# Kernel tuning notes

Hardware: AMD Instinct MI355X
Metric: run time of the kernel (lower is better)

## Reference

```python
import jax, jax.numpy as jnp
import numpy as np

PAD, BOS, EOS, UNK = 0, 1, 2, 3
B, S, V, D, L = 256, 512, 50000, 256, 128

def setup_inputs() -> dict:
    key = jax.random.key(0)
    ks = jax.random.split(key, 12)
    vocab_tensor = jax.random.randint(ks[0], (B, S), 4, V)
    parent_idx = jax.random.randint(ks[1], (B, S), 0, S)
    pbond = jax.random.randint(ks[2], (B, S), 0, 4)
    bond = jax.random.randint(ks[3], (B, S), 0, 4)
    patom = jax.random.randint(ks[4], (B, S), 0, 16)
    atom = jax.random.randint(ks[5], (B, S), 0, 16)
    btype = jax.random.randint(ks[6], (B, S), 0, 4)
    order_tensor = jnp.stack([parent_idx, pbond, bond, patom, atom, btype], axis=-1)
    lengths = jax.random.randint(ks[7], (B,), 1, S + 1)
    mask_tensor = jnp.arange(S)[None, :] < lengths[:, None]  # ragged prefix masks
    eps = jax.random.normal(ks[8], (B, L), dtype=jnp.float32)
    sc = 1.0 / np.sqrt(D)
    emb = jax.random.normal(ks[9], (V, D), dtype=jnp.float32) * sc
    Wm = jax.random.normal(ks[10], (D, L), dtype=jnp.float32) * sc
    Wv = jax.random.normal(ks[11], (D, L), dtype=jnp.float32) * sc
    Wlin = jax.random.normal(jax.random.fold_in(key, 20), (L, D), dtype=jnp.float32) / np.sqrt(L)
    Wout = jax.random.normal(jax.random.fold_in(key, 21), (D, D), dtype=jnp.float32) * sc
    return {
        'vocab_tensor': vocab_tensor, 'order_tensor': order_tensor, 'mask_tensor': mask_tensor,
        'eps': eps, 'emb': emb, 'Wm': Wm, 'bm': jnp.zeros((L,), jnp.float32),
        'Wv': Wv, 'bv': jnp.zeros((L,), jnp.float32), 'Wlin': Wlin,
        'blin': jnp.zeros((D,), jnp.float32), 'Wout': Wout, 'bout': jnp.zeros((D,), jnp.float32),
    }

def _forward(vocab_tensor, order_tensor, mask_tensor, eps, emb, Wm, bm, Wv, bv, Wlin, blin, Wout, bout):
    # --- mask bond-pos columns (torch.where assignments, vectorized) ---
    # (columns 1 and 2 set to -1 where masked; kept implicitly via vt/pad handling)
    # --- calc_chem_z path: masked vocab, parent gather, edge one-hot ---
    vt = jnp.where(mask_tensor, vocab_tensor, PAD)                      # [B,S]
    vocab_emb = emb[vt]                                                 # [B,S,D]
    oi = order_tensor[..., 0]
    oi = jnp.where(oi == -1, BOS, oi)
    parent = jnp.where(mask_tensor, jnp.take_along_axis(vt, oi, axis=1), PAD)
    parent = parent.at[:, 0].set(BOS)
    parent_emb = emb[parent]                                            # [B,S,D]
    idx = jnp.clip(order_tensor[..., 5] - 1, -1, None)
    edge_type = jnp.where((idx >= 0)[..., None],
                          jax.nn.one_hot(jnp.clip(idx, 0), 3, dtype=jnp.float32), 0.0)  # [B,S,3]
    # pooling stand-in for (undefined) StructureEncoder -> [B,D]
    m = mask_tensor[..., None].astype(jnp.float32)
    enc = ((vocab_emb + parent_emb) * m).sum(1) / jnp.maximum(m.sum(1), 1.0)
    enc = enc * (1.0 + 0.0 * edge_type.sum())  # keep edge_type in graph
    # --- LatentSampler ---
    mean = enc @ Wm + bm
    log_var = enc @ Wv + bv
    z = mean + eps * jnp.exp(0.5 * log_var)
    memory = z @ Wlin + blin                                            # [B,D]
    # --- vectorized bos/eos/pad sequence assembly (the hot loop in torch) ---
    inp = jnp.concatenate([jnp.full((B, 1), BOS, vocab_tensor.dtype), vocab_tensor], axis=1)  # [B,S+1]
    mask_ex = jnp.concatenate([jnp.ones((B, 1), bool), mask_tensor], axis=1)
    tgt = jnp.roll(inp, -1, axis=1)
    first_false = jnp.argmax(~mask_ex, axis=1)                          # first eos position
    has_false = jnp.any(~mask_ex, axis=1)
    pos = jnp.arange(S + 1)[None, :]
    tgt = jnp.where(has_false[:, None] & (pos == first_false[:, None] - 1), EOS, tgt)
    kill = has_false[:, None] & (pos >= first_false[:, None])
    tgt = jnp.where(kill, PAD, tgt)
    inp = jnp.where(kill, PAD, inp)
    # edge_index assembly (faithful, consumed by decoder in original)
    padneg = jnp.full((B, 1), -1, order_tensor.dtype)
    edge_index = jnp.concatenate([padneg, jnp.where(mask_tensor, order_tensor[..., 0], -2) + 1], axis=1)
    # --- embedding lookups + decoder stand-in + output head ---
    node_embed = emb[inp]                                               # [B,S+1,D]
    dec = node_embed + memory[:, None, :]
    dec = dec + 0.0 * edge_index[..., None].astype(jnp.float32)         # keep edge_index in graph
    word_emb = dec @ Wout + bout
    tgt_emb = emb[tgt]
    valid = (tgt != PAD)
    sq = (word_emb - tgt_emb) ** 2 * valid[..., None]
    token_loss = sq.sum() / jnp.maximum(valid.sum() * D, 1).astype(jnp.float32)
    kl = -0.5 * jnp.sum(1.0 + log_var - mean ** 2 - jnp.exp(log_var)) / B
    return token_loss, kl

def reference(vocab_tensor, order_tensor, mask_tensor, eps, emb, Wm, bm, Wv, bv, Wlin, blin, Wout, bout):
    return _forward(vocab_tensor, order_tensor, mask_tensor, eps, emb, Wm, bm, Wv, bv, Wlin, blin, Wout, bout)
```

## Files before the change

kernel.cpp:

```cpp
#include <hip/hip_runtime.h>

#define B_ 256
#define S_ 512
#define V_ 50000
#define D_ 256
#define L_ 128
#define PGRID 512

typedef __attribute__((ext_vector_type(8))) short short8;
typedef __attribute__((ext_vector_type(4))) float floatx4;

#define OFF_SQP  16
#define OFF_WT   (OFF_SQP + 256)
#define OFF_EB   (OFF_WT + 32768)
#define OFF_P    (OFF_EB + (V_ * D_ / 2))

__device__ __forceinline__ unsigned short f2bf(float x) {
    unsigned u = __float_as_uint(x);
    u += 0x7FFFu + ((u >> 16) & 1u);
    return (unsigned short)(u >> 16);
}
__device__ __forceinline__ float bf2f(unsigned short u) {
    return __uint_as_float(((unsigned)u) << 16);
}

__global__ __launch_bounds__(256) void prep_kernel(const float* __restrict__ emb,
                                                   const float* __restrict__ Wout,
                                                   unsigned short* __restrict__ embb,
                                                   unsigned short* __restrict__ Wt,
                                                   float* __restrict__ ws) {
    __shared__ float sT[64][65];
    const int tid = threadIdx.x;
    if (blockIdx.x == 0) {
        if (tid < 16) ((int*)ws)[tid] = 0;
        ws[OFF_SQP + tid] = 0.f;
    }
    if (blockIdx.x < 16) {
        const int bx = blockIdx.x;
        const int k0 = (bx & 3) * 64, n0 = (bx >> 2) * 64;
        const int c = tid & 63, rg = tid >> 6;
#pragma unroll
        for (int i = 0; i < 16; ++i) {
            int r = rg * 16 + i;
            sT[c][r] = Wout[(k0 + r) * D_ + n0 + c];
        }
        __syncthreads();
#pragma unroll
        for (int i = 0; i < 16; ++i) {
            int r = rg * 16 + i;
            Wt[(size_t)(n0 + r) * D_ + k0 + c] = f2bf(sT[r][c]);
        }
    }
    const int N4 = V_ * D_ / 4;
    for (int i = blockIdx.x * 256 + tid; i < N4; i += gridDim.x * 256) {
        float4 v = ((const float4*)emb)[i];
        ushort4 h;
        h.x = f2bf(v.x); h.y = f2bf(v.y); h.z = f2bf(v.z); h.w = f2bf(v.w);
        ((ushort4*)embb)[i] = h;
    }
}

__global__ __launch_bounds__(256, 2) void pgemm_kernel(
    const unsigned short* __restrict__ embb, const unsigned short* __restrict__ Wt,
    unsigned short* __restrict__ P) {
    const int tid = threadIdx.x;
    const int wv = tid >> 6, lane = tid & 63;
    const int lo = lane & 15, hi = lane >> 4;
    const int NCH = V_ / 16;

    short8 bfr[4][8];
    const unsigned short* wbase = Wt + (size_t)(wv * 64 + lo) * D_ + hi * 8;
#pragma unroll
    for (int nt = 0; nt < 4; ++nt)
#pragma unroll
        for (int kk = 0; kk < 8; ++kk)
            bfr[nt][kk] = *(const short8*)(wbase + nt * 16 * D_ + kk * 32);

    int ch = blockIdx.x;
    const unsigned short* abase = embb + (size_t)(ch * 16 + lo) * D_ + hi * 8;
    short8 acur[8];
#pragma unroll
    for (int kk = 0; kk < 8; ++kk) acur[kk] = *(const short8*)(abase + kk * 32);

    for (; ch < NCH; ch += PGRID) {
        const int chn = (ch + PGRID < NCH) ? (ch + PGRID) : ch;
        const unsigned short* anext = embb + (size_t)(chn * 16 + lo) * D_ + hi * 8;
        short8 anxt[8];
#pragma unroll
        for (int kk = 0; kk < 8; ++kk) anxt[kk] = *(const short8*)(anext + kk * 32);

        floatx4 acc[4];
#pragma unroll
        for (int nt = 0; nt < 4; ++nt) acc[nt] = (floatx4){0.f, 0.f, 0.f, 0.f};
#pragma unroll
        for (int kk = 0; kk < 8; ++kk)
#pragma unroll
            for (int nt = 0; nt < 4; ++nt)
                acc[nt] = __builtin_amdgcn_mfma_f32_16x16x32_bf16(
                    acur[kk], bfr[nt][kk], acc[nt], 0, 0, 0);

#pragma unroll
        for (int r = 0; r < 4; ++r) {
            unsigned short* prow = P + (size_t)(ch * 16 + hi * 4 + r) * D_ + wv * 64 + lo;
#pragma unroll
            for (int nt = 0; nt < 4; ++nt) prow[nt * 16] = f2bf(acc[nt][r]);
        }
#pragma unroll
        for (int kk = 0; kk < 8; ++kk) acur[kk] = anxt[kk];
    }
}

__global__ __launch_bounds__(1024) void enclat_kernel(
    const int* __restrict__ vocab, const int* __restrict__ order,
    const int* __restrict__ mask, const unsigned short* __restrict__ embb,
    const unsigned short* __restrict__ P, const float* __restrict__ eps,
    const float* __restrict__ Wm, const float* __restrict__ bm,
    const float* __restrict__ Wv, const float* __restrict__ bv,
    const float* __restrict__ Wlin, const float* __restrict__ blin,
    const float* __restrict__ Wout, const float* __restrict__ bout,
    float* __restrict__ ws, float* __restrict__ out) {
    __shared__ int s_id1[S_], s_id2[S_];
    __shared__ float4 s_part[15 * 64];
    __shared__ float s_enc[D_];
    __shared__ float s_mean[L_], s_lv[L_], s_z[L_], s_mem[D_], s_Q[D_];
    __shared__ float s_red[256];
    __shared__ float s_wred[16];
    __shared__ int s_cnt, s_prev;
    const int b = blockIdx.x;
    const int tid = threadIdx.x;
    float* kl_acc = ws + 1;
    int* vc_acc = (int*)ws + 2;
    int* done = (int*)ws + 3;
    float* sqp = ws + OFF_SQP;

    if (tid == 0) s_cnt = 0;
    __syncthreads();
    if (tid < S_) {
        int j = tid;
        int mk = mask[b * S_ + j];
        int id1 = 0, id2 = 0;
        if (mk) {
            id1 = vocab[b * S_ + j];
            if (j == 0) {
                id2 = 1;
            } else {
                int oi = order[(size_t)(b * S_ + j) * 6];
                if (oi == -1) oi = 1;
                id2 = mask[b * S_ + oi] ? vocab[b * S_ + oi] : 0;
            }
        }
        s_id1[j] = id1;
        s_id2[j] = id2;
        unsigned long long bal = __ballot(mk != 0);
        if ((tid & 63) == 0) atomicAdd(&s_cnt, __popcll(bal));
    }
    __syncthreads();
    const int cnt = s_cnt;
    const int jg = tid >> 6, d4 = tid & 63;
    const ushort4* eb4 = (const ushort4*)embb;
    float4 a = {0.f, 0.f, 0.f, 0.f};
#pragma unroll 8
    for (int j = jg; j < cnt; j += 16) {
        ushort4 x = eb4[(size_t)s_id1[j] * 64 + d4];
        ushort4 y = eb4[(size_t)s_id2[j] * 64 + d4];
        a.x += bf2f(x.x) + bf2f(y.x);
        a.y += bf2f(x.y) + bf2f(y.y);
        a.z += bf2f(x.z) + bf2f(y.z);
        a.w += bf2f(x.w) + bf2f(y.w);
    }
    if (jg) s_part[(jg - 1) * 64 + d4] = a;
    __syncthreads();
    if (jg == 0) {
#pragma unroll
        for (int g = 0; g < 15; ++g) {
            float4 p = s_part[g * 64 + d4];
            a.x += p.x; a.y += p.y; a.z += p.z; a.w += p.w;
        }
        float inv = 1.f / fmaxf((float)cnt, 1.f);
        a.x *= inv; a.y *= inv; a.z *= inv; a.w *= inv;
        ((float4*)s_enc)[d4] = a;
    }
    __syncthreads();
    float dot = 0.f;
    if (tid < 256) {
        const int l = tid & (L_ - 1);
        const float* W = (tid < L_) ? Wm : Wv;
        const float* bb = (tid < L_) ? bm : bv;
        dot = bb[l];
        for (int d = 0; d < D_; ++d) dot = fmaf(s_enc[d], W[d * L_ + l], dot);
        if (tid < L_) s_mean[l] = dot; else s_lv[l] = dot;
    }
    __syncthreads();
    float klp = 0.f;
    if (tid < L_) {
        float mn = s_mean[tid], lv = s_lv[tid];
        s_z[tid] = mn + eps[b * L_ + tid] * expf(0.5f * lv);
        klp = 1.f + lv - mn * mn - expf(lv);
    }
    if (tid < 256) s_red[tid] = klp;
    __syncthreads();
    for (int s = 128; s > 0; s >>= 1) {
        if (tid < s) s_red[tid] += s_red[tid + s];
        __syncthreads();
    }
    const float kl_part = s_red[0];
    if (tid < 256) {
        float mem = blin[tid];
        for (int l2 = 0; l2 < L_; ++l2) mem = fmaf(s_z[l2], Wlin[l2 * D_ + tid], mem);
        s_mem[tid] = mem;
    }
    __syncthreads();
    if (tid < 256) {
        float qv = bout[tid];
        for (int k = 0; k < D_; ++k) qv = fmaf(s_mem[k], Wout[k * D_ + tid], qv);
        s_Q[tid] = qv;
    }
    __syncthreads();
    const int lane = tid & 63;
    const int c = lane * 4;
    const float4 q4 = *(const float4*)(s_Q + c);
    float acc = 0.f;
    for (int j0 = jg * 4; j0 <= cnt; j0 += 64) {
        int inp[4], tgt[4];
        float wgt[4];
#pragma unroll
        for (int u = 0; u < 4; ++u) {
            const int j = j0 + u;
            const bool v = (j <= cnt);
            const int jc = v ? j : 0;
            inp[u] = (jc == 0) ? 1 : s_id1[jc - 1];
            tgt[u] = v ? ((j < cnt) ? s_id1[j] : ((cnt < S_) ? 2 : 1)) : 1;
            wgt[u] = v ? 1.f : 0.f;
        }
        ushort4 pv[4], tv[4];
#pragma unroll
        for (int u = 0; u < 4; ++u) {
            pv[u] = *(const ushort4*)(P + (size_t)inp[u] * D_ + c);
            tv[u] = *(const ushort4*)(embb + (size_t)tgt[u] * D_ + c);
        }
#pragma unroll
        for (int u = 0; u < 4; ++u) {
            float d0 = bf2f(pv[u].x) + q4.x - bf2f(tv[u].x);
            float d1 = bf2f(pv[u].y) + q4.y - bf2f(tv[u].y);
            float d2 = bf2f(pv[u].z) + q4.z - bf2f(tv[u].z);
            float d3 = bf2f(pv[u].w) + q4.w - bf2f(tv[u].w);
            float s = fmaf(d0, d0, fmaf(d1, d1, fmaf(d2, d2, d3 * d3)));
            acc = fmaf(wgt[u], s, acc);
        }
    }
#pragma unroll
    for (int off = 32; off; off >>= 1) acc += __shfl_down(acc, off, 64);
    if (lane == 0) s_wred[jg] = acc;
    __syncthreads();
    if (tid == 0) {
        float tot = 0.f;
#pragma unroll
        for (int g = 0; g < 16; ++g) tot += s_wred[g];
        sqp[b] = tot;
        atomicAdd(kl_acc, kl_part);
        atomicAdd(vc_acc, cnt + 1);
        __threadfence();
        s_prev = atomicAdd(done, 1);
    }
    __syncthreads();
    if (s_prev == B_ - 1) {
        float v = (tid < 256) ? atomicAdd(&sqp[tid], 0.f) : 0.f;
        if (tid < 256) s_red[tid] = v;
        __syncthreads();
        for (int s = 128; s > 0; s >>= 1) {
            if (tid < s) s_red[tid] += s_red[tid + s];
            __syncthreads();
        }
        if (tid == 0) {
            float kl = atomicAdd(kl_acc, 0.f);
            int vc = atomicAdd(vc_acc, 0);
            long long denom = (long long)vc * D_;
            if (denom < 1) denom = 1;
            out[0] = s_red[0] / (float)denom;
            out[1] = -0.5f * kl / (float)B_;
        }
    }
}

extern "C" void kernel_launch(void* const* d_in, const int* in_sizes, int n_in,
                              void* d_out, int out_size, void* d_ws, size_t ws_size,
                              hipStream_t stream) {
    const int* vocab = (const int*)d_in[0];
    const int* order = (const int*)d_in[1];
    const int* mask  = (const int*)d_in[2];
    const float* eps  = (const float*)d_in[3];
    const float* emb  = (const float*)d_in[4];
    const float* Wm   = (const float*)d_in[5];
    const float* bm   = (const float*)d_in[6];
    const float* Wv   = (const float*)d_in[7];
    const float* bv   = (const float*)d_in[8];
    const float* Wlin = (const float*)d_in[9];
    const float* blin = (const float*)d_in[10];
    const float* Wout = (const float*)d_in[11];
    const float* bout = (const float*)d_in[12];

    float* ws = (float*)d_ws;
    unsigned short* Wt = (unsigned short*)(ws + OFF_WT);
    unsigned short* embb = (unsigned short*)(ws + OFF_EB);
    unsigned short* P = (unsigned short*)(ws + OFF_P);

    prep_kernel<<<2048, 256, 0, stream>>>(emb, Wout, embb, Wt, ws);
    pgemm_kernel<<<PGRID, 256, 0, stream>>>(embb, Wt, P);
    enclat_kernel<<<B_, 1024, 0, stream>>>(vocab, order, mask, embb, P, eps,
                                           Wm, bm, Wv, bv, Wlin, blin, Wout, bout,
                                           ws, (float*)d_out);
}
```

Before: 178.3 us.

## Fuse embedding GEMM with encoder in one launch and split loss scan across blocks

Result: slower. 270.9 us (+52.0%).

```diff
diff --git a/kernel.cpp b/kernel.cpp
--- a/kernel.cpp
+++ b/kernel.cpp
@@ -5,15 +5,20 @@
 #define V_ 50000
 #define D_ 256
 #define L_ 128
-#define PGRID 512
+#define NG 512
+#define NENC 256
+#define NCH (V_ / 16)
+#define NSPLIT 8
+#define K2B (B_ * NSPLIT)
 
 typedef __attribute__((ext_vector_type(8))) short short8;
 typedef __attribute__((ext_vector_type(4))) float floatx4;
 
-#define OFF_SQP  16
-#define OFF_WT   (OFF_SQP + 256)
-#define OFF_EB   (OFF_WT + 32768)
-#define OFF_P    (OFF_EB + (V_ * D_ / 2))
+#define OFF_SQP 16
+#define OFF_KL  (OFF_SQP + 256)
+#define OFF_CNT (OFF_KL + 256)
+#define OFF_Q   (OFF_CNT + 256)
+#define OFF_P   (OFF_Q + B_ * D_)
 
 __device__ __forceinline__ unsigned short f2bf(float x) {
     unsigned u = __float_as_uint(x);
@@ -23,121 +28,87 @@
 __device__ __forceinline__ float bf2f(unsigned short u) {
     return __uint_as_float(((unsigned)u) << 16);
 }
-
-__global__ __launch_bounds__(256) void prep_kernel(const float* __restrict__ emb,
-                                                   const float* __restrict__ Wout,
-                                                   unsigned short* __restrict__ embb,
-                                                   unsigned short* __restrict__ Wt,
-                                                   float* __restrict__ ws) {
-    __shared__ float sT[64][65];
+__device__ __forceinline__ short8 cvt8(float4 a, float4 b) {
+    short8 r;
+    r[0] = (short)f2bf(a.x); r[1] = (short)f2bf(a.y);
+    r[2] = (short)f2bf(a.z); r[3] = (short)f2bf(a.w);
+    r[4] = (short)f2bf(b.x); r[5] = (short)f2bf(b.y);
+    r[6] = (short)f2bf(b.z); r[7] = (short)f2bf(b.w);
+    return r;
+}
+
+__global__ __launch_bounds__(512, 4) void fused1(
+    const int* __restrict__ vocab, const int* __restrict__ order,
+    const int* __restrict__ mask, const float* __restrict__ emb,
+    const float* __restrict__ eps, const float* __restrict__ Wm,
+    const float* __restrict__ bm, const float* __restrict__ Wv,
+    const float* __restrict__ bv, const float* __restrict__ Wlin,
+    const float* __restrict__ blin, const float* __restrict__ Wout,
+    const float* __restrict__ bout, float* __restrict__ ws) {
     const int tid = threadIdx.x;
-    if (blockIdx.x == 0) {
-        if (tid < 16) ((int*)ws)[tid] = 0;
-        ws[OFF_SQP + tid] = 0.f;
-    }
-    if (blockIdx.x < 16) {
-        const int bx = blockIdx.x;
-        const int k0 = (bx & 3) * 64, n0 = (bx >> 2) * 64;
-        const int c = tid & 63, rg = tid >> 6;
-#pragma unroll
-        for (int i = 0; i < 16; ++i) {
-            int r = rg * 16 + i;
-            sT[c][r] = Wout[(k0 + r) * D_ + n0 + c];
-        }
-        __syncthreads();
-#pragma unroll
-        for (int i = 0; i < 16; ++i) {
-            int r = rg * 16 + i;
-            Wt[(size_t)(n0 + r) * D_ + k0 + c] = f2bf(sT[r][c]);
-        }
-    }
-    const int N4 = V_ * D_ / 4;
-    for (int i = blockIdx.x * 256 + tid; i < N4; i += gridDim.x * 256) {
-        float4 v = ((const float4*)emb)[i];
-        ushort4 h;
-        h.x = f2bf(v.x); h.y = f2bf(v.y); h.z = f2bf(v.z); h.w = f2bf(v.w);
-        ((ushort4*)embb)[i] = h;
-    }
-}
-
-__global__ __launch_bounds__(256, 2) void pgemm_kernel(
-    const unsigned short* __restrict__ embb, const unsigned short* __restrict__ Wt,
-    unsigned short* __restrict__ P) {
-    const int tid = threadIdx.x;
-    const int wv = tid >> 6, lane = tid & 63;
-    const int lo = lane & 15, hi = lane >> 4;
-    const int NCH = V_ / 16;
-
-    short8 bfr[4][8];
-    const unsigned short* wbase = Wt + (size_t)(wv * 64 + lo) * D_ + hi * 8;
-#pragma unroll
-    for (int nt = 0; nt < 4; ++nt)
-#pragma unroll
-        for (int kk = 0; kk < 8; ++kk)
-            bfr[nt][kk] = *(const short8*)(wbase + nt * 16 * D_ + kk * 32);
-
-    int ch = blockIdx.x;
-    const unsigned short* abase = embb + (size_t)(ch * 16 + lo) * D_ + hi * 8;
-    short8 acur[8];
-#pragma unroll
-    for (int kk = 0; kk < 8; ++kk) acur[kk] = *(const short8*)(abase + kk * 32);
-
-    for (; ch < NCH; ch += PGRID) {
-        const int chn = (ch + PGRID < NCH) ? (ch + PGRID) : ch;
-        const unsigned short* anext = embb + (size_t)(chn * 16 + lo) * D_ + hi * 8;
-        short8 anxt[8];
-#pragma unroll
-        for (int kk = 0; kk < 8; ++kk) anxt[kk] = *(const short8*)(anext + kk * 32);
-
-        floatx4 acc[4];
-#pragma unroll
-        for (int nt = 0; nt < 4; ++nt) acc[nt] = (floatx4){0.f, 0.f, 0.f, 0.f};
-#pragma unroll
-        for (int kk = 0; kk < 8; ++kk)
-#pragma unroll
-            for (int nt = 0; nt < 4; ++nt)
-                acc[nt] = __builtin_amdgcn_mfma_f32_16x16x32_bf16(
-                    acur[kk], bfr[nt][kk], acc[nt], 0, 0, 0);
-
-#pragma unroll
-        for (int r = 0; r < 4; ++r) {
-            unsigned short* prow = P + (size_t)(ch * 16 + hi * 4 + r) * D_ + wv * 64 + lo;
-#pragma unroll
-            for (int nt = 0; nt < 4; ++nt) prow[nt * 16] = f2bf(acc[nt][r]);
-        }
-#pragma unroll
-        for (int kk = 0; kk < 8; ++kk) acur[kk] = anxt[kk];
-    }
-}
-
-__global__ __launch_bounds__(1024) void enclat_kernel(
-    const int* __restrict__ vocab, const int* __restrict__ order,
-    const int* __restrict__ mask, const unsigned short* __restrict__ embb,
-    const unsigned short* __restrict__ P, const float* __restrict__ eps,
-    const float* __restrict__ Wm, const float* __restrict__ bm,
-    const float* __restrict__ Wv, const float* __restrict__ bv,
-    const float* __restrict__ Wlin, const float* __restrict__ blin,
-    const float* __restrict__ Wout, const float* __restrict__ bout,
-    float* __restrict__ ws, float* __restrict__ out) {
+    if (blockIdx.x >= NENC) {
+        const int gb = blockIdx.x - NENC;
+        if (gb == 0 && tid == 0) ((int*)ws)[3] = 0;
+        unsigned short* __restrict__ P = (unsigned short*)(ws + OFF_P);
+        const int lane = tid & 63;
+        const int wv = tid >> 6;
+        const int lo = lane & 15, hi = lane >> 4;
+        const int colbase = wv * 32;
+        short8 bfr[2][8];
+#pragma unroll
+        for (int nt = 0; nt < 2; ++nt)
+#pragma unroll
+            for (int kk = 0; kk < 8; ++kk) {
+                const float* wp = Wout + (size_t)(hi * 8 + kk * 32) * D_ +
+                                  colbase + nt * 16 + lo;
+                short8 w;
+#pragma unroll
+                for (int e = 0; e < 8; ++e) w[e] = (short)f2bf(wp[(size_t)e * D_]);
+                bfr[nt][kk] = w;
+            }
+        for (int ch = gb; ch < NCH; ch += NG) {
+            const float* abase = emb + (size_t)(ch * 16 + lo) * D_ + hi * 8;
+            floatx4 acc0 = {0.f, 0.f, 0.f, 0.f}, acc1 = {0.f, 0.f, 0.f, 0.f};
+#pragma unroll
+            for (int kh = 0; kh < 2; ++kh) {
+                float4 t0[4], t1[4];
+#pragma unroll
+                for (int q = 0; q < 4; ++q) {
+                    const float* ap = abase + (kh * 4 + q) * 32;
+                    t0[q] = *(const float4*)ap;
+                    t1[q] = *(const float4*)(ap + 4);
+                }
+#pragma unroll
+                for (int q = 0; q < 4; ++q) {
+                    short8 av = cvt8(t0[q], t1[q]);
+                    acc0 = __builtin_amdgcn_mfma_f32_16x16x32_bf16(
+                        av, bfr[0][kh * 4 + q], acc0, 0, 0, 0);
+                    acc1 = __builtin_amdgcn_mfma_f32_16x16x32_bf16(
+                        av, bfr[1][kh * 4 + q], acc1, 0, 0, 0);
+                }
+            }
+#pragma unroll
+            for (int r = 0; r < 4; ++r) {
+                unsigned short* prow =
+                    P + (size_t)(ch * 16 + hi * 4 + r) * D_ + colbase + lo;
+                prow[0] = f2bf(acc0[r]);
+                prow[16] = f2bf(acc1[r]);
+            }
+        }
+        return;
+    }
     __shared__ int s_id1[S_], s_id2[S_];
-    __shared__ float4 s_part[15 * 64];
+    __shared__ float4 s_part[7 * 64];
     __shared__ float s_enc[D_];
-    __shared__ float s_mean[L_], s_lv[L_], s_z[L_], s_mem[D_], s_Q[D_];
+    __shared__ float s_mean[L_], s_lv[L_], s_z[L_], s_mem[D_];
     __shared__ float s_red[256];
-    __shared__ float s_wred[16];
-    __shared__ int s_cnt, s_prev;
+    __shared__ int s_cnt;
     const int b = blockIdx.x;
-    const int tid = threadIdx.x;
-    float* kl_acc = ws + 1;
-    int* vc_acc = (int*)ws + 2;
-    int* done = (int*)ws + 3;
-    float* sqp = ws + OFF_SQP;
-
     if (tid == 0) s_cnt = 0;
     __syncthreads();
-    if (tid < S_) {
-        int j = tid;
-        int mk = mask[b * S_ + j];
+    {
+        const int j = tid;
+        const int mk = mask[b * S_ + j];
         int id1 = 0, id2 = 0;
         if (mk) {
             id1 = vocab[b * S_ + j];
@@ -157,36 +128,33 @@
     __syncthreads();
     const int cnt = s_cnt;
     const int jg = tid >> 6, d4 = tid & 63;
-    const ushort4* eb4 = (const ushort4*)embb;
+    const float4* eb4 = (const float4*)emb;
     float4 a = {0.f, 0.f, 0.f, 0.f};
-#pragma unroll 8
-    for (int j = jg; j < cnt; j += 16) {
-        ushort4 x = eb4[(size_t)s_id1[j] * 64 + d4];
-        ushort4 y = eb4[(size_t)s_id2[j] * 64 + d4];
-        a.x += bf2f(x.x) + bf2f(y.x);
-        a.y += bf2f(x.y) + bf2f(y.y);
-        a.z += bf2f(x.z) + bf2f(y.z);
-        a.w += bf2f(x.w) + bf2f(y.w);
+#pragma unroll 4
+    for (int j = jg; j < cnt; j += 8) {
+        float4 x = eb4[(size_t)s_id1[j] * 64 + d4];
+        float4 y = eb4[(size_t)s_id2[j] * 64 + d4];
+        a.x += x.x + y.x; a.y += x.y + y.y;
+        a.z += x.z + y.z; a.w += x.w + y.w;
     }
     if (jg) s_part[(jg - 1) * 64 + d4] = a;
     __syncthreads();
     if (jg == 0) {
 #pragma unroll
-        for (int g = 0; g < 15; ++g) {
+        for (int g = 0; g < 7; ++g) {
             float4 p = s_part[g * 64 + d4];
             a.x += p.x; a.y += p.y; a.z += p.z; a.w += p.w;
         }
-        float inv = 1.f / fmaxf((float)cnt, 1.f);
+        const float inv = 1.f / fmaxf((float)cnt, 1.f);
         a.x *= inv; a.y *= inv; a.z *= inv; a.w *= inv;
         ((float4*)s_enc)[d4] = a;
     }
     __syncthreads();
-    float dot = 0.f;
     if (tid < 256) {
         const int l = tid & (L_ - 1);
         const float* W = (tid < L_) ? Wm : Wv;
         const float* bb = (tid < L_) ? bm : bv;
-        dot = bb[l];
+        float dot = bb[l];
         for (int d = 0; d < D_; ++d) dot = fmaf(s_enc[d], W[d * L_ + l], dot);
         if (tid < L_) s_mean[l] = dot; else s_lv[l] = dot;
     }
@@ -203,7 +171,11 @@
         if (tid < s) s_red[tid] += s_red[tid + s];
         __syncthreads();
     }
-    const float kl_part = s_red[0];
+    if (tid == 0) {
+        ws[OFF_KL + b] = s_red[0];
+        ((int*)ws)[OFF_CNT + b] = cnt;
+        ws[OFF_SQP + b] = 0.f;
+    }
     if (tid < 256) {
         float mem = blin[tid];
         for (int l2 = 0; l2 < L_; ++l2) mem = fmaf(s_z[l2], Wlin[l2 * D_ + tid], mem);
@@ -213,71 +185,103 @@
     if (tid < 256) {
         float qv = bout[tid];
         for (int k = 0; k < D_; ++k) qv = fmaf(s_mem[k], Wout[k * D_ + tid], qv);
-        s_Q[tid] = qv;
-    }
-    __syncthreads();
-    const int lane = tid & 63;
-    const int c = lane * 4;
-    const float4 q4 = *(const float4*)(s_Q + c);
+        ws[OFF_Q + b * D_ + tid] = qv;
+    }
+}
+
+__global__ __launch_bounds__(256) void scan2(const int* __restrict__ vocab,
+                                             const float* __restrict__ emb,
+                                             float* __restrict__ ws,
+                                             float* __restrict__ out) {
+    __shared__ int s_sid[80];
+    __shared__ float s_wred[4];
+    __shared__ float s_red[256];
+    __shared__ int s_prev;
+    const int tid = threadIdx.x;
+    const int b = blockIdx.x >> 3, part = blockIdx.x & 7;
+    const unsigned short* __restrict__ P = (const unsigned short*)(ws + OFF_P);
+    float* sqp = ws + OFF_SQP;
+    int* done = (int*)ws + 3;
+    const int cnt = ((const int*)ws)[OFF_CNT + b];
+    const int npos = cnt + 1;
+    const int per = (npos + NSPLIT - 1) / NSPLIT;
+    const int j0 = part * per;
+    const int jend = min(j0 + per, npos);
+    const int lo_s = (j0 > 0) ? j0 - 1 : 0;
+    const int nstage = min(jend, cnt) - lo_s;
+    if (tid < nstage) s_sid[tid] = vocab[b * S_ + lo_s + tid];
+    __syncthreads();
+    const int jgq = tid >> 6, lane = tid & 63, c = lane * 4;
+    const float4 q4 = *(const float4*)(ws + OFF_Q + b * D_ + c);
     float acc = 0.f;
-    for (int j0 = jg * 4; j0 <= cnt; j0 += 64) {
+    for (int jj = j0 + jgq * 4; jj < jend; jj += 16) {
         int inp[4], tgt[4];
         float wgt[4];
 #pragma unroll
         for (int u = 0; u < 4; ++u) {
-            const int j = j0 + u;
-            const bool v = (j <= cnt);
-            const int jc = v ? j : 0;
-            inp[u] = (jc == 0) ? 1 : s_id1[jc - 1];
-            tgt[u] = v ? ((j < cnt) ? s_id1[j] : ((cnt < S_) ? 2 : 1)) : 1;
+            const int j = jj + u;
+            const bool v = (j < jend);
+            const int jc = v ? j : jj;
+            inp[u] = (jc == 0) ? 1 : s_sid[jc - 1 - lo_s];
+            tgt[u] = (jc < cnt) ? s_sid[jc - lo_s] : ((cnt < S_) ? 2 : 1);
             wgt[u] = v ? 1.f : 0.f;
         }
-        ushort4 pv[4], tv[4];
+        ushort4 pv[4];
+        float4 tv[4];
 #pragma unroll
         for (int u = 0; u < 4; ++u) {
             pv[u] = *(const ushort4*)(P + (size_t)inp[u] * D_ + c);
-            tv[u] = *(const ushort4*)(embb + (size_t)tgt[u] * D_ + c);
+            tv[u] = *(const float4*)(emb + (size_t)tgt[u] * D_ + c);
         }
 #pragma unroll
         for (int u = 0; u < 4; ++u) {
-            float d0 = bf2f(pv[u].x) + q4.x - bf2f(tv[u].x);
-            float d1 = bf2f(pv[u].y) + q4.y - bf2f(tv[u].y);
-            float d2 = bf2f(pv[u].z) + q4.z - bf2f(tv[u].z);
-            float d3 = bf2f(pv[u].w) + q4.w - bf2f(tv[u].w);
+            float d0 = bf2f(pv[u].x) + q4.x - tv[u].x;
+            float d1 = bf2f(pv[u].y) + q4.y - tv[u].y;
+            float d2 = bf2f(pv[u].z) + q4.z - tv[u].z;
+            float d3 = bf2f(pv[u].w) + q4.w - tv[u].w;
             float s = fmaf(d0, d0, fmaf(d1, d1, fmaf(d2, d2, d3 * d3)));
             acc = fmaf(wgt[u], s, acc);
         }
     }
 #pragma unroll
     for (int off = 32; off; off >>= 1) acc += __shfl_down(acc, off, 64);
-    if (lane == 0) s_wred[jg] = acc;
+    if (lane == 0) s_wred[jgq] = acc;
     __syncthreads();
     if (tid == 0) {
-        float tot = 0.f;
-#pragma unroll
-        for (int g = 0; g < 16; ++g) tot += s_wred[g];
-        sqp[b] = tot;
-        atomicAdd(kl_acc, kl_part);
-        atomicAdd(vc_acc, cnt + 1);
+        float tot = s_wred[0] + s_wred[1] + s_wred[2] + s_wred[3];
+        atomicAdd(&sqp[b], tot);
         __threadfence();
         s_prev = atomicAdd(done, 1);
     }
     __syncthreads();
-    if (s_prev == B_ - 1) {
-        float v = (tid < 256) ? atomicAdd(&sqp[tid], 0.f) : 0.f;
-        if (tid < 256) s_red[tid] = v;
+    if (s_prev == K2B - 1) {
+        s_red[tid] = atomicAdd(&sqp[tid], 0.f);
         __syncthreads();
         for (int s = 128; s > 0; s >>= 1) {
             if (tid < s) s_red[tid] += s_red[tid + s];
             __syncthreads();
         }
+        const float sq_tot = s_red[0];
+        __syncthreads();
+        s_red[tid] = ws[OFF_KL + tid];
+        __syncthreads();
+        for (int s = 128; s > 0; s >>= 1) {
+            if (tid < s) s_red[tid] += s_red[tid + s];
+            __syncthreads();
+        }
+        const float kl_tot = s_red[0];
+        __syncthreads();
+        s_red[tid] = (float)(((const int*)ws)[OFF_CNT + tid] + 1);
+        __syncthreads();
+        for (int s = 128; s > 0; s >>= 1) {
+            if (tid < s) s_red[tid] += s_red[tid + s];
+            __syncthreads();
+        }
         if (tid == 0) {
-            float kl = atomicAdd(kl_acc, 0.f);
-            int vc = atomicAdd(vc_acc, 0);
-            long long denom = (long long)vc * D_;
-            if (denom < 1) denom = 1;
-            out[0] = s_red[0] / (float)denom;
-            out[1] = -0.5f * kl / (float)B_;
+            float denom = s_red[0] * (float)D_;
+            if (denom < 1.f) denom = 1.f;
+            out[0] = sq_tot / denom;
+            out[1] = -0.5f * kl_tot / (float)B_;
         }
     }
 }
@@ -300,13 +304,7 @@
     const float* bout = (const float*)d_in[12];
 
     float* ws = (float*)d_ws;
-    unsigned short* Wt = (unsigned short*)(ws + OFF_WT);
-    unsigned short* embb = (unsigned short*)(ws + OFF_EB);
-    unsigned short* P = (unsigned short*)(ws + OFF_P);
-
-    prep_kernel<<<2048, 256, 0, stream>>>(emb, Wout, embb, Wt, ws);
-    pgemm_kernel<<<PGRID, 256, 0, stream>>>(embb, Wt, P);
-    enclat_kernel<<<B_, 1024, 0, stream>>>(vocab, order, mask, embb, P, eps,
-                                           Wm, bm, Wv, bv, Wlin, blin, Wout, bout,
-                                           ws, (float*)d_out);
-}
+    fused1<<<NENC + NG, 512, 0, stream>>>(vocab, order, mask, emb, eps, Wm, bm,
+                                          Wv, bv, Wlin, blin, Wout, bout, ws);
+    scan2<<<K2B, 256, 0, stream>>>(vocab, emb, ws, (float*)d_out);
+}
```
